# Kernel optimization log

Measured on AMD Instinct MI355X. Metric: run time of the kernel, lower is better.

## Reference

```python
import jax, jax.numpy as jnp
import numpy as np

N, E = 100000, 1600000
D_IN, D_H, D_OUT = 32, 64, 1


def _init_linear(key, fan_in, fan_out):
    k1, k2 = jax.random.split(key)
    lim = 1.0 / np.sqrt(fan_in)
    w = jax.random.uniform(k1, (fan_in, fan_out), minval=-lim, maxval=lim, dtype=jnp.float32)
    b = jax.random.uniform(k2, (fan_out,), minval=-lim, maxval=lim, dtype=jnp.float32)
    return w, b


def setup_inputs() -> dict:
    key = jax.random.key(0)
    ks = jax.random.split(key, 8)
    x = jax.random.normal(ks[0], (N, D_IN), dtype=jnp.float32)
    edge_index = jax.random.randint(ks[1], (2, E), 0, N, dtype=jnp.int64)
    w1_rel, b1 = _init_linear(ks[2], D_IN, D_H)
    w1_root, _ = _init_linear(ks[3], D_IN, D_H)
    w2_rel, b2 = _init_linear(ks[4], D_H, D_H)
    w2_root, _ = _init_linear(ks[5], D_H, D_H)
    w3_rel, b3 = _init_linear(ks[6], D_H, D_OUT)
    w3_root, _ = _init_linear(ks[7], D_H, D_OUT)
    return {
        "x": x,
        "w1_rel": w1_rel, "b1": b1, "w1_root": w1_root,
        "w2_rel": w2_rel, "b2": b2, "w2_root": w2_root,
        "w3_rel": w3_rel, "b3": b3, "w3_root": w3_root,
        "edge_index": edge_index,
    }


def _graph_conv(x, edge_index, w_rel, b_rel, w_root):
    # PyG GraphConv: out_i = W_rel @ (sum_{j->i} x_j) + b_rel + W_root @ x_i
    src, dst = edge_index[0], edge_index[1]
    agg = jax.ops.segment_sum(x[src], dst, num_segments=x.shape[0])  # [N, d]
    return agg @ w_rel + b_rel + x @ w_root


def reference(x, w1_rel, b1, w1_root, w2_rel, b2, w2_root, w3_rel, b3, w3_root, edge_index):
    # Dropout is inactive in eval mode (F.dropout with training=False is identity).
    h = jax.nn.relu(_graph_conv(x, edge_index, w1_rel, b1, w1_root))
    h = jax.nn.relu(_graph_conv(h, edge_index, w2_rel, b2, w2_root))
    out = _graph_conv(h, edge_index, w3_rel, b3, w3_root)
    return out.reshape(-1)  # [N], since output_dim == 1
```

## Files before the change

### kernel.cpp

```cpp
#include <hip/hip_runtime.h>
#include <hip/hip_fp16.h>

typedef _Float16 f16x8 __attribute__((ext_vector_type(8)));
typedef float    f32x4 __attribute__((ext_vector_type(4)));

constexpr int DIN = 32;
constexpr int DH  = 64;
constexpr int NBSHIFT = 8;
constexpr int TILE_A  = 4096;
constexpr int FB_CAP  = 6144;

__global__ __launch_bounds__(256) void k_prep(
    const int* __restrict__ dst, const float2* __restrict__ x2,
    __half2* __restrict__ xh,
    const float* __restrict__ w1_rel, const float* __restrict__ w1_root,
    const float* __restrict__ w2_rel, const float* __restrict__ w2_root,
    __half* __restrict__ wf1, __half* __restrict__ wf2,
    int* __restrict__ ch, int E, int n2, int nbuckets) {
  __shared__ int hist[512];
  int tid = threadIdx.x, b = blockIdx.x;
  long long t0 = (long long)b * TILE_A;
  int cnt = (int)min((long long)TILE_A, (long long)E - t0);
  if (cnt < 0) cnt = 0;
  for (int i = tid; i < 512; i += 256) hist[i] = 0;
  __syncthreads();
  for (int r = tid; r < cnt; r += 256)
    atomicAdd(&hist[dst[t0 + r] >> NBSHIFT], 1);
  __syncthreads();
  for (int i = tid; i < nbuckets; i += 256)
    if (hist[i]) atomicAdd(&ch[i], hist[i]);
  for (int i = b * 256 + tid; i < n2; i += gridDim.x * 256) {
    float2 v = x2[i];
    xh[i] = __floats2half2_rn(v.x, v.y);
  }
  if (b == 1) {
    for (int u = tid; u < 512; u += 256) {
      int lane = u & 63, kt = (u >> 6) & 1, mt = u >> 7;
      int outc = 16 * mt + (lane & 15);
      int kb = 32 * kt + (lane >> 4) * 8;
      union { uint4 q; __half h[8]; } w;
#pragma unroll
      for (int j = 0; j < 8; ++j) {
        int k = kb + j;
        float wv = (k < 32) ? w1_root[k * DH + outc] : w1_rel[(k - 32) * DH + outc];
        w.h[j] = __float2half(wv);
      }
      *(uint4*)(wf1 + (size_t)u * 8) = w.q;
    }
  } else if (b == 2) {
    for (int u = tid; u < 1024; u += 256) {
      int lane = u & 63, kt = (u >> 6) & 3, mt = u >> 8;
      int outc = 16 * mt + (lane & 15);
      int kb = 32 * kt + (lane >> 4) * 8;
      union { uint4 q; __half h[8]; } w;
#pragma unroll
      for (int j = 0; j < 8; ++j) {
        int k = kb + j;
        float wv = (k < 64) ? w2_rel[k * DH + outc] : w2_root[(k - 64) * DH + outc];
        w.h[j] = __float2half(wv);
      }
      *(uint4*)(wf2 + (size_t)u * 8) = w.q;
    }
  }
}

__global__ __launch_bounds__(256) void k_cscan(
    const int* __restrict__ ch, int* __restrict__ cb, int* __restrict__ bcur,
    int nbuckets, int E) {
  __shared__ int ts[256];
  int tid = threadIdx.x;
  int i0 = tid * 2, i1 = i0 + 1;
  int v0 = (i0 < nbuckets) ? ch[i0] : 0;
  int v1 = (i1 < nbuckets) ? ch[i1] : 0;
  int s = v0 + v1;
  ts[tid] = s;
  __syncthreads();
  for (int off = 1; off < 256; off <<= 1) {
    int val = (tid >= off) ? ts[tid - off] : 0;
    __syncthreads();
    ts[tid] += val;
    __syncthreads();
  }
  int ex = ts[tid] - s;
  if (i0 < nbuckets) { cb[i0] = ex;      bcur[i0] = ex; }
  if (i1 < nbuckets) { cb[i1] = ex + v0; bcur[i1] = ex + v0; }
  if (tid == 255) cb[nbuckets] = E;
}

__global__ __launch_bounds__(256) void k_binA(
    const int* __restrict__ src, const int* __restrict__ dst,
    int* __restrict__ bcur, unsigned* __restrict__ bin,
    int E, int nbuckets) {
  __shared__ int hist[512];
  __shared__ int lbase[512];
  __shared__ int gbase[512];
  __shared__ int ts[256];
  __shared__ unsigned lsort[TILE_A];
  __shared__ unsigned short lbuck[TILE_A];
  long long t0 = (long long)blockIdx.x * TILE_A;
  int cnt = (int)min((long long)TILE_A, (long long)E - t0);
  for (int i = threadIdx.x; i < 512; i += 256) hist[i] = 0;
  __syncthreads();
  unsigned pk[TILE_A / 256];
  int bo[TILE_A / 256];
#pragma unroll
  for (int q = 0; q < TILE_A / 256; ++q) {
    int r = (int)threadIdx.x + q * 256;
    if (r < cnt) {
      int d = dst[t0 + r];
      int s = src[t0 + r];
      int b = d >> NBSHIFT;
      int off = atomicAdd(&hist[b], 1);
      pk[q] = ((unsigned)(d & 255) << 17) | (unsigned)s;
      bo[q] = (b << 16) | off;
    }
  }
  __syncthreads();
  {
    int i0 = threadIdx.x * 2, i1 = i0 + 1;
    int v0 = hist[i0], v1 = hist[i1];
    int s2 = v0 + v1;
    ts[threadIdx.x] = s2;
    __syncthreads();
    for (int off = 1; off < 256; off <<= 1) {
      int val = (threadIdx.x >= off) ? ts[threadIdx.x - off] : 0;
      __syncthreads();
      ts[threadIdx.x] += val;
      __syncthreads();
    }
    int ex = ts[threadIdx.x] - s2;
    lbase[i0] = ex;
    lbase[i1] = ex + v0;
    gbase[i0] = v0 ? atomicAdd(&bcur[i0], v0) : 0;
    gbase[i1] = v1 ? atomicAdd(&bcur[i1], v1) : 0;
  }
  __syncthreads();
#pragma unroll
  for (int q = 0; q < TILE_A / 256; ++q) {
    int r = (int)threadIdx.x + q * 256;
    if (r < cnt) {
      int b = bo[q] >> 16, off = bo[q] & 0xFFFF;
      int li = lbase[b] + off;
      lsort[li] = pk[q];
      lbuck[li] = (unsigned short)b;
    }
  }
  __syncthreads();
  for (int i = threadIdx.x; i < cnt; i += 256) {
    int b = lbuck[i];
    bin[gbase[b] + (i - lbase[b])] = lsort[i];
  }
}

__global__ __launch_bounds__(256) void k_fillB_l1(
    const unsigned* __restrict__ bin, const int* __restrict__ cb,
    int* __restrict__ rp, int* __restrict__ ssrc,
    const _Float16* __restrict__ X, const _Float16* __restrict__ WF1,
    const float* __restrict__ b1, _Float16* __restrict__ H1, int n, int E) {
  __shared__ int deg[256];
  __shared__ int ts[256];
  __shared__ int cur[256];
  __shared__ int ubuf[FB_CAP];
  __shared__ _Float16 sagg[64 * 40];
  int b = blockIdx.x;
  int tid = threadIdx.x;
  int nbase = b << NBSHIFT;
  int nn = min(256, n - nbase);
  int ebeg = cb[b], eend = cb[b + 1];
  int cnt = eend - ebeg;
  deg[tid] = 0;
  __syncthreads();
  for (int e = ebeg + tid; e < eend; e += 256)
    atomicAdd(&deg[bin[e] >> 17], 1);
  __syncthreads();
  int d = deg[tid];
  ts[tid] = d;
  __syncthreads();
  for (int off = 1; off < 256; off <<= 1) {
    int val = (tid >= off) ? ts[tid - off] : 0;
    __syncthreads();
    ts[tid] += val;
    __syncthreads();
  }
  int pref = ts[tid] - d;
  if (tid < nn) rp[nbase + tid] = ebeg + pref;
  if (b == 0 && tid == 0) rp[n] = E;
  cur[tid] = pref;
  __syncthreads();
  bool fit = (cnt <= FB_CAP);
  if (fit) {
    for (int e = ebeg + tid; e < eend; e += 256) {
      unsigned u = bin[e];
      int pos = atomicAdd(&cur[u >> 17], 1);
      ubuf[pos] = (int)(u & 0x1FFFF);
    }
    __syncthreads();
    for (int i = tid; i < cnt; i += 256)
      ssrc[ebeg + i] = ubuf[i];
  } else {
    for (int e = ebeg + tid; e < eend; e += 256) {
      unsigned u = bin[e];
      int pos = atomicAdd(&cur[u >> 17], 1);
      ssrc[ebeg + pos] = (int)(u & 0x1FFFF);
    }
    __syncthreads();
  }
  __syncthreads();

  const f16x8* fx = (const f16x8*)X;
  int lane = tid & 63;
  int w = tid >> 6;
  for (int sub = 0; sub < 4; ++sub) {
    int nl = tid >> 2;
    int unit = tid & 3;
    int ln = sub * 64 + nl;
    {
      f16x8 accA = (f16x8)(_Float16)0.0f;
      f16x8 accB = (f16x8)(_Float16)0.0f;
      if (ln < nn) {
        int beg = ts[ln] - deg[ln];
        int end = ts[ln];
        int e = beg;
        if (fit) {
          for (; e + 7 < end; e += 8) {
            int s0 = ubuf[e],     s1 = ubuf[e + 1], s2 = ubuf[e + 2], s3 = ubuf[e + 3];
            int s4 = ubuf[e + 4], s5 = ubuf[e + 5], s6 = ubuf[e + 6], s7 = ubuf[e + 7];
            f16x8 v0 = fx[(size_t)s0 * 4 + unit];
            f16x8 v1 = fx[(size_t)s1 * 4 + unit];
            f16x8 v2 = fx[(size_t)s2 * 4 + unit];
            f16x8 v3 = fx[(size_t)s3 * 4 + unit];
            f16x8 v4 = fx[(size_t)s4 * 4 + unit];
            f16x8 v5 = fx[(size_t)s5 * 4 + unit];
            f16x8 v6 = fx[(size_t)s6 * 4 + unit];
            f16x8 v7 = fx[(size_t)s7 * 4 + unit];
            accA += v0; accB += v1; accA += v2; accB += v3;
            accA += v4; accB += v5; accA += v6; accB += v7;
          }
          for (; e + 1 < end; e += 2) {
            f16x8 v0 = fx[(size_t)ubuf[e] * 4 + unit];
            f16x8 v1 = fx[(size_t)ubuf[e + 1] * 4 + unit];
            accA += v0; accB += v1;
          }
          if (e < end) accA += fx[(size_t)ubuf[e] * 4 + unit];
        } else {
          const int* gs = ssrc + ebeg;
          for (; e + 1 < end; e += 2) {
            f16x8 v0 = fx[(size_t)gs[e] * 4 + unit];
            f16x8 v1 = fx[(size_t)gs[e + 1] * 4 + unit];
            accA += v0; accB += v1;
          }
          if (e < end) accA += fx[(size_t)gs[e] * 4 + unit];
        }
      }
      *(f16x8*)&sagg[nl * 40 + unit * 8] = accA + accB;
    }
    __syncthreads();
    int nl16 = w * 16 + (lane & 15);
    int node = nbase + sub * 64 + nl16;
    int nodeld = min(node, n - 1);
    f16x8 bf0 = *(const f16x8*)(X + (size_t)nodeld * 32 + (lane >> 4) * 8);
    f16x8 bf1 = *(const f16x8*)&sagg[nl16 * 40 + (lane >> 4) * 8];
    const f16x8* ap = (const f16x8*)WF1 + lane;
    f32x4 acc[4];
#pragma unroll
    for (int mt = 0; mt < 4; ++mt) acc[mt] = (f32x4)(0.f);
#pragma unroll
    for (int mt = 0; mt < 4; ++mt) {
      acc[mt] = __builtin_amdgcn_mfma_f32_16x16x32_f16(ap[(mt * 2 + 0) * 64], bf0, acc[mt], 0, 0, 0);
      acc[mt] = __builtin_amdgcn_mfma_f32_16x16x32_f16(ap[(mt * 2 + 1) * 64], bf1, acc[mt], 0, 0, 0);
    }
    if (node < n) {
      int jb = (lane >> 4) * 4;
      _Float16* op = H1 + (size_t)node * 64 + jb;
#pragma unroll
      for (int mt = 0; mt < 4; ++mt) {
        f32x4 vb = *(const f32x4*)(b1 + 16 * mt + jb);
        union { uint2 u2; _Float16 h[4]; } pko;
#pragma unroll
        for (int r = 0; r < 4; ++r)
          pko.h[r] = (_Float16)fmaxf(acc[mt][r] + vb[r], 0.f);
        *(uint2*)(op + 16 * mt) = pko.u2;
      }
    }
    __syncthreads();
  }
}

__global__ __launch_bounds__(256) void k_l2fused(
    const _Float16* __restrict__ H1, const int* __restrict__ rp,
    const int* __restrict__ ssrc, const _Float16* __restrict__ WF,
    const float* __restrict__ b2, const float* __restrict__ w3rel,
    const float* __restrict__ w3root,
    float* __restrict__ S, float* __restrict__ T, int n) {
  __shared__ _Float16 sagg[64][72];
  int tid = threadIdx.x;
  int nl = tid >> 2;
  int u0 = tid & 3;
  int nodeg = blockIdx.x * 64 + nl;
  {
    f16x8 aA = (f16x8)(_Float16)0.0f, aB = (f16x8)(_Float16)0.0f;
    f16x8 cA = (f16x8)(_Float16)0.0f, cB = (f16x8)(_Float16)0.0f;
    if (nodeg < n) {
      int beg = rp[nodeg], end = rp[nodeg + 1];
      const f16x8* fh = (const f16x8*)H1;
      int e = beg;
      for (; e + 7 < end; e += 8) {
        int s0 = ssrc[e],     s1 = ssrc[e + 1], s2 = ssrc[e + 2], s3 = ssrc[e + 3];
        int s4 = ssrc[e + 4], s5 = ssrc[e + 5], s6 = ssrc[e + 6], s7 = ssrc[e + 7];
        f16x8 a0 = fh[(size_t)s0 * 8 + u0];
        f16x8 c0 = fh[(size_t)s0 * 8 + u0 + 4];
        f16x8 a1 = fh[(size_t)s1 * 8 + u0];
        f16x8 c1 = fh[(size_t)s1 * 8 + u0 + 4];
        f16x8 a2 = fh[(size_t)s2 * 8 + u0];
        f16x8 c2 = fh[(size_t)s2 * 8 + u0 + 4];
        f16x8 a3 = fh[(size_t)s3 * 8 + u0];
        f16x8 c3 = fh[(size_t)s3 * 8 + u0 + 4];
        f16x8 a4 = fh[(size_t)s4 * 8 + u0];
        f16x8 c4 = fh[(size_t)s4 * 8 + u0 + 4];
        f16x8 a5 = fh[(size_t)s5 * 8 + u0];
        f16x8 c5 = fh[(size_t)s5 * 8 + u0 + 4];
        f16x8 a6 = fh[(size_t)s6 * 8 + u0];
        f16x8 c6 = fh[(size_t)s6 * 8 + u0 + 4];
        f16x8 a7 = fh[(size_t)s7 * 8 + u0];
        f16x8 c7 = fh[(size_t)s7 * 8 + u0 + 4];
        aA += a0; cA += c0; aB += a1; cB += c1;
        aA += a2; cA += c2; aB += a3; cB += c3;
        aA += a4; cA += c4; aB += a5; cB += c5;
        aA += a6; cA += c6; aB += a7; cB += c7;
      }
      for (; e + 1 < end; e += 2) {
        int s0 = ssrc[e], s1 = ssrc[e + 1];
        aA += fh[(size_t)s0 * 8 + u0];
        cA += fh[(size_t)s0 * 8 + u0 + 4];
        aB += fh[(size_t)s1 * 8 + u0];
        cB += fh[(size_t)s1 * 8 + u0 + 4];
      }
      if (e < end) {
        int s0 = ssrc[e];
        aA += fh[(size_t)s0 * 8 + u0];
        cA += fh[(size_t)s0 * 8 + u0 + 4];
      }
    }
    *(f16x8*)&sagg[nl][u0 * 8] = aA + aB;
    *(f16x8*)&sagg[nl][(u0 + 4) * 8] = cA + cB;
  }
  __syncthreads();
  int lane = tid & 63;
  int w = tid >> 6;
  int nl16 = w * 16 + (lane & 15);
  int node = blockIdx.x * 64 + nl16;
  int nodeld = min(node, n - 1);
  f16x8 bf[4];
  bf[0] = *(const f16x8*)&sagg[nl16][(lane >> 4) * 8];
  bf[1] = *(const f16x8*)&sagg[nl16][32 + (lane >> 4) * 8];
  bf[2] = *(const f16x8*)(H1 + (size_t)nodeld * 64 + (lane >> 4) * 8);
  bf[3] = *(const f16x8*)(H1 + (size_t)nodeld * 64 + 32 + (lane >> 4) * 8);
  const f16x8* ap = (const f16x8*)WF + lane;
  f32x4 acc[4];
#pragma unroll
  for (int mt = 0; mt < 4; ++mt) acc[mt] = (f32x4)(0.f);
#pragma unroll
  for (int mt = 0; mt < 4; ++mt)
#pragma unroll
    for (int kt = 0; kt < 4; ++kt)
      acc[mt] = __builtin_amdgcn_mfma_f32_16x16x32_f16(
          ap[(mt * 4 + kt) * 64], bf[kt], acc[mt], 0, 0, 0);
  int jb = (lane >> 4) * 4;
  float s = 0.f, t = 0.f;
#pragma unroll
  for (int mt = 0; mt < 4; ++mt) {
    f32x4 vb = *(const f32x4*)(b2 + 16 * mt + jb);
    f32x4 vr = *(const f32x4*)(w3rel + 16 * mt + jb);
    f32x4 vt = *(const f32x4*)(w3root + 16 * mt + jb);
#pragma unroll
    for (int r = 0; r < 4; ++r) {
      float h = fmaxf(acc[mt][r] + vb[r], 0.f);
      s = fmaf(h, vr[r], s);
      t = fmaf(h, vt[r], t);
    }
  }
  s += __shfl_xor(s, 16); s += __shfl_xor(s, 32);
  t += __shfl_xor(t, 16); t += __shfl_xor(t, 32);
  if (lane < 16 && node < n) { S[node] = s; T[node] = t; }
}

__global__ __launch_bounds__(256) void k_final(
    const float* __restrict__ sv, const int* __restrict__ rp,
    const int* __restrict__ ssrc, const float* __restrict__ T,
    const float* __restrict__ b3, float* __restrict__ out, int n) {
  int t = blockIdx.x * 256 + threadIdx.x;
  int node = t >> 2;
  int l = t & 3;
  if (node >= n) return;
  int beg = rp[node], end = rp[node + 1];
  float a = 0.f;
  for (int e = beg + l; e < end; e += 4) a += sv[ssrc[e]];
  a += __shfl_xor(a, 1);
  a += __shfl_xor(a, 2);
  if (l == 0) out[node] = a + b3[0] + T[node];
}


extern "C" void kernel_launch(void* const* d_in, const int* in_sizes, int n_in,
                              void* d_out, int out_size, void* d_ws, size_t ws_size,
                              hipStream_t stream) {
  const float* x       = (const float*)d_in[0];
  const float* w1_rel  = (const float*)d_in[1];
  const float* b1      = (const float*)d_in[2];
  const float* w1_root = (const float*)d_in[3];
  const float* w2_rel  = (const float*)d_in[4];
  const float* b2      = (const float*)d_in[5];
  const float* w2_root = (const float*)d_in[6];
  const float* w3_rel  = (const float*)d_in[7];
  const float* b3      = (const float*)d_in[8];
  const float* w3_root = (const float*)d_in[9];
  const int*   edge    = (const int*)d_in[10];

  const int n = in_sizes[0] / DIN;
  const int E = in_sizes[10] / 2;
  const int* src = edge;
  const int* dst = edge + E;

  _Float16* XH = (_Float16*)d_ws;
  _Float16* H1 = XH + (size_t)n * 32;
  float*    S  = (float*)(H1 + (size_t)n * 64);
  float*    T  = S + n;
  int* RP   = (int*)(T + n);
  int* SSRC = RP + ((n + 8) & ~7);
  unsigned* BIN = (unsigned*)(SSRC + E);
  int* CH   = (int*)(BIN + E);
  int* CB   = CH + 512;
  int* BCUR = CB + 520;
  __half* WF1 = (__half*)(BCUR + 512);
  __half* WF2 = WF1 + 4096;

  const int B = 256;
  const int nbuckets = (n + 255) >> NBSHIFT;
  const int ntiles = (E + TILE_A - 1) / TILE_A;
  const int gF = (n + 63) / 64;
  int n2 = n * 16;

  hipMemsetAsync(CH, 0, 512 * sizeof(int), stream);
  k_prep<<<ntiles, B, 0, stream>>>(dst, (const float2*)x, (__half2*)XH,
                                   w1_rel, w1_root, w2_rel, w2_root,
                                   WF1, WF2, CH, E, n2, nbuckets);
  k_cscan<<<1, B, 0, stream>>>(CH, CB, BCUR, nbuckets, E);
  k_binA<<<ntiles, B, 0, stream>>>(src, dst, BCUR, BIN, E, nbuckets);
  k_fillB_l1<<<nbuckets, B, 0, stream>>>(BIN, CB, RP, SSRC,
                                         XH, (const _Float16*)WF1, b1, H1, n, E);
  k_l2fused<<<gF, B, 0, stream>>>(H1, RP, SSRC, (const _Float16*)WF2,
                                  b2, w3_rel, w3_root, S, T, n);
  k_final<<<(4 * n + B - 1) / B, B, 0, stream>>>(S, RP, SSRC, T, b3, (float*)d_out, n);
}
```

Before: 138.5 us.

## Split CSR fill from layer-1 aggregation into separate kernel with more blocks

```diff
diff --git a/kernel.cpp b/kernel.cpp
--- a/kernel.cpp
+++ b/kernel.cpp
@@ -152,16 +152,13 @@
   }
 }
 
-__global__ __launch_bounds__(256) void k_fillB_l1(
+__global__ __launch_bounds__(256) void k_fillB(
     const unsigned* __restrict__ bin, const int* __restrict__ cb,
-    int* __restrict__ rp, int* __restrict__ ssrc,
-    const _Float16* __restrict__ X, const _Float16* __restrict__ WF1,
-    const float* __restrict__ b1, _Float16* __restrict__ H1, int n, int E) {
+    int* __restrict__ rp, int* __restrict__ ssrc, int n, int E) {
   __shared__ int deg[256];
   __shared__ int ts[256];
   __shared__ int cur[256];
-  __shared__ int ubuf[FB_CAP];
-  __shared__ _Float16 sagg[64 * 40];
+  __shared__ int lsort[FB_CAP];
   int b = blockIdx.x;
   int tid = threadIdx.x;
   int nbase = b << NBSHIFT;
@@ -187,102 +184,91 @@
   if (b == 0 && tid == 0) rp[n] = E;
   cur[tid] = pref;
   __syncthreads();
-  bool fit = (cnt <= FB_CAP);
-  if (fit) {
+  if (cnt <= FB_CAP) {
     for (int e = ebeg + tid; e < eend; e += 256) {
       unsigned u = bin[e];
       int pos = atomicAdd(&cur[u >> 17], 1);
-      ubuf[pos] = (int)(u & 0x1FFFF);
+      lsort[pos] = (int)(u & 0x1FFFF);
     }
     __syncthreads();
     for (int i = tid; i < cnt; i += 256)
-      ssrc[ebeg + i] = ubuf[i];
+      ssrc[ebeg + i] = lsort[i];
   } else {
     for (int e = ebeg + tid; e < eend; e += 256) {
       unsigned u = bin[e];
       int pos = atomicAdd(&cur[u >> 17], 1);
       ssrc[ebeg + pos] = (int)(u & 0x1FFFF);
     }
-    __syncthreads();
-  }
-  __syncthreads();
-
-  const f16x8* fx = (const f16x8*)X;
+  }
+}
+
+__global__ __launch_bounds__(256) void k_l1fused(
+    const _Float16* __restrict__ X, const int* __restrict__ rp,
+    const int* __restrict__ ssrc, const _Float16* __restrict__ WF,
+    const float* __restrict__ b1, _Float16* __restrict__ H1, int n) {
+  __shared__ _Float16 sagg[64][40];
+  int tid = threadIdx.x;
+  int nl = tid >> 2;
+  int unit = tid & 3;
+  int nodeg = blockIdx.x * 64 + nl;
+  {
+    f16x8 accA = (f16x8)(_Float16)0.0f;
+    f16x8 accB = (f16x8)(_Float16)0.0f;
+    if (nodeg < n) {
+      int beg = rp[nodeg], end = rp[nodeg + 1];
+      const f16x8* fx = (const f16x8*)X;
+      int e = beg;
+      for (; e + 7 < end; e += 8) {
+        int s0 = ssrc[e],     s1 = ssrc[e + 1], s2 = ssrc[e + 2], s3 = ssrc[e + 3];
+        int s4 = ssrc[e + 4], s5 = ssrc[e + 5], s6 = ssrc[e + 6], s7 = ssrc[e + 7];
+        f16x8 v0 = fx[(size_t)s0 * 4 + unit];
+        f16x8 v1 = fx[(size_t)s1 * 4 + unit];
+        f16x8 v2 = fx[(size_t)s2 * 4 + unit];
+        f16x8 v3 = fx[(size_t)s3 * 4 + unit];
+        f16x8 v4 = fx[(size_t)s4 * 4 + unit];
+        f16x8 v5 = fx[(size_t)s5 * 4 + unit];
+        f16x8 v6 = fx[(size_t)s6 * 4 + unit];
+        f16x8 v7 = fx[(size_t)s7 * 4 + unit];
+        accA += v0; accB += v1; accA += v2; accB += v3;
+        accA += v4; accB += v5; accA += v6; accB += v7;
+      }
+      for (; e + 1 < end; e += 2) {
+        f16x8 v0 = fx[(size_t)ssrc[e] * 4 + unit];
+        f16x8 v1 = fx[(size_t)ssrc[e + 1] * 4 + unit];
+        accA += v0; accB += v1;
+      }
+      if (e < end) accA += fx[(size_t)ssrc[e] * 4 + unit];
+    }
+    *(f16x8*)&sagg[nl][unit * 8] = accA + accB;
+  }
+  __syncthreads();
   int lane = tid & 63;
   int w = tid >> 6;
-  for (int sub = 0; sub < 4; ++sub) {
-    int nl = tid >> 2;
-    int unit = tid & 3;
-    int ln = sub * 64 + nl;
-    {
-      f16x8 accA = (f16x8)(_Float16)0.0f;
-      f16x8 accB = (f16x8)(_Float16)0.0f;
-      if (ln < nn) {
-        int beg = ts[ln] - deg[ln];
-        int end = ts[ln];
-        int e = beg;
-        if (fit) {
-          for (; e + 7 < end; e += 8) {
-            int s0 = ubuf[e],     s1 = ubuf[e + 1], s2 = ubuf[e + 2], s3 = ubuf[e + 3];
-            int s4 = ubuf[e + 4], s5 = ubuf[e + 5], s6 = ubuf[e + 6], s7 = ubuf[e + 7];
-            f16x8 v0 = fx[(size_t)s0 * 4 + unit];
-            f16x8 v1 = fx[(size_t)s1 * 4 + unit];
-            f16x8 v2 = fx[(size_t)s2 * 4 + unit];
-            f16x8 v3 = fx[(size_t)s3 * 4 + unit];
-            f16x8 v4 = fx[(size_t)s4 * 4 + unit];
-            f16x8 v5 = fx[(size_t)s5 * 4 + unit];
-            f16x8 v6 = fx[(size_t)s6 * 4 + unit];
-            f16x8 v7 = fx[(size_t)s7 * 4 + unit];
-            accA += v0; accB += v1; accA += v2; accB += v3;
-            accA += v4; accB += v5; accA += v6; accB += v7;
-          }
-          for (; e + 1 < end; e += 2) {
-            f16x8 v0 = fx[(size_t)ubuf[e] * 4 + unit];
-            f16x8 v1 = fx[(size_t)ubuf[e + 1] * 4 + unit];
-            accA += v0; accB += v1;
-          }
-          if (e < end) accA += fx[(size_t)ubuf[e] * 4 + unit];
-        } else {
-          const int* gs = ssrc + ebeg;
-          for (; e + 1 < end; e += 2) {
-            f16x8 v0 = fx[(size_t)gs[e] * 4 + unit];
-            f16x8 v1 = fx[(size_t)gs[e + 1] * 4 + unit];
-            accA += v0; accB += v1;
-          }
-          if (e < end) accA += fx[(size_t)gs[e] * 4 + unit];
-        }
-      }
-      *(f16x8*)&sagg[nl * 40 + unit * 8] = accA + accB;
-    }
-    __syncthreads();
-    int nl16 = w * 16 + (lane & 15);
-    int node = nbase + sub * 64 + nl16;
-    int nodeld = min(node, n - 1);
-    f16x8 bf0 = *(const f16x8*)(X + (size_t)nodeld * 32 + (lane >> 4) * 8);
-    f16x8 bf1 = *(const f16x8*)&sagg[nl16 * 40 + (lane >> 4) * 8];
-    const f16x8* ap = (const f16x8*)WF1 + lane;
-    f32x4 acc[4];
-#pragma unroll
-    for (int mt = 0; mt < 4; ++mt) acc[mt] = (f32x4)(0.f);
-#pragma unroll
-    for (int mt = 0; mt < 4; ++mt) {
-      acc[mt] = __builtin_amdgcn_mfma_f32_16x16x32_f16(ap[(mt * 2 + 0) * 64], bf0, acc[mt], 0, 0, 0);
-      acc[mt] = __builtin_amdgcn_mfma_f32_16x16x32_f16(ap[(mt * 2 + 1) * 64], bf1, acc[mt], 0, 0, 0);
-    }
-    if (node < n) {
-      int jb = (lane >> 4) * 4;
-      _Float16* op = H1 + (size_t)node * 64 + jb;
-#pragma unroll
-      for (int mt = 0; mt < 4; ++mt) {
-        f32x4 vb = *(const f32x4*)(b1 + 16 * mt + jb);
-        union { uint2 u2; _Float16 h[4]; } pko;
-#pragma unroll
-        for (int r = 0; r < 4; ++r)
-          pko.h[r] = (_Float16)fmaxf(acc[mt][r] + vb[r], 0.f);
-        *(uint2*)(op + 16 * mt) = pko.u2;
-      }
-    }
-    __syncthreads();
+  int nl16 = w * 16 + (lane & 15);
+  int node = blockIdx.x * 64 + nl16;
+  int nodeld = min(node, n - 1);
+  f16x8 bf0 = *(const f16x8*)(X + (size_t)nodeld * 32 + (lane >> 4) * 8);
+  f16x8 bf1 = *(const f16x8*)&sagg[nl16][(lane >> 4) * 8];
+  const f16x8* ap = (const f16x8*)WF + lane;
+  f32x4 acc[4];
+#pragma unroll
+  for (int mt = 0; mt < 4; ++mt) acc[mt] = (f32x4)(0.f);
+#pragma unroll
+  for (int mt = 0; mt < 4; ++mt) {
+    acc[mt] = __builtin_amdgcn_mfma_f32_16x16x32_f16(ap[(mt * 2 + 0) * 64], bf0, acc[mt], 0, 0, 0);
+    acc[mt] = __builtin_amdgcn_mfma_f32_16x16x32_f16(ap[(mt * 2 + 1) * 64], bf1, acc[mt], 0, 0, 0);
+  }
+  if (node >= n) return;
+  int jb = (lane >> 4) * 4;
+  _Float16* op = H1 + (size_t)node * 64 + jb;
+#pragma unroll
+  for (int mt = 0; mt < 4; ++mt) {
+    f32x4 vb = *(const f32x4*)(b1 + 16 * mt + jb);
+    union { uint2 u2; _Float16 h[4]; } pko;
+#pragma unroll
+    for (int r = 0; r < 4; ++r)
+      pko.h[r] = (_Float16)fmaxf(acc[mt][r] + vb[r], 0.f);
+    *(uint2*)(op + 16 * mt) = pko.u2;
   }
 }
 
@@ -446,8 +432,8 @@
                                    WF1, WF2, CH, E, n2, nbuckets);
   k_cscan<<<1, B, 0, stream>>>(CH, CB, BCUR, nbuckets, E);
   k_binA<<<ntiles, B, 0, stream>>>(src, dst, BCUR, BIN, E, nbuckets);
-  k_fillB_l1<<<nbuckets, B, 0, stream>>>(BIN, CB, RP, SSRC,
-                                         XH, (const _Float16*)WF1, b1, H1, n, E);
+  k_fillB<<<nbuckets, B, 0, stream>>>(BIN, CB, RP, SSRC, n, E);
+  k_l1fused<<<gF, B, 0, stream>>>(XH, RP, SSRC, (const _Float16*)WF1, b1, H1, n);
   k_l2fused<<<gF, B, 0, stream>>>(H1, RP, SSRC, (const _Float16*)WF2,
                                   b2, w3_rel, w3_root, S, T, n);
   k_final<<<(4 * n + B - 1) / B, B, 0, stream>>>(S, RP, SSRC, T, b3, (float*)d_out, n);
```

Result: no change. 140.7 us (+1.6%).
